# Kernel tuning notes

Measured on AMD Instinct MI355X. Metric: run time of the kernel, lower is better.

## Reference

```python
import jax, jax.numpy as jnp
import numpy as np

N = 65536
H = 512
E = 8
OUT = 2

def setup_inputs() -> dict:
    key = jax.random.key(0)
    ks = jax.random.split(key, 9)
    s = 0.1
    return {
        "x": jax.random.normal(ks[0], (N, 10), dtype=jnp.float32),
        "w1": jax.random.normal(ks[1], (H,), dtype=jnp.float32) * s,        # fc1: Linear(1,H) weight
        "b1": jax.random.normal(ks[2], (H,), dtype=jnp.float32) * s,
        "meta_w": jax.random.normal(ks[3], (E, H), dtype=jnp.float32) * s,  # 8 Linear(1,H) weights stacked
        "meta_b": jax.random.normal(ks[4], (E, H), dtype=jnp.float32) * s,
        "w2": jax.random.normal(ks[5], (H, H), dtype=jnp.float32) * s,      # fc2 weight (in,out layout)
        "b2": jax.random.normal(ks[6], (H,), dtype=jnp.float32) * s,
        "w3": jax.random.normal(ks[7], (H, OUT), dtype=jnp.float32) * s,    # fc3 weight
        "b3": jax.random.normal(ks[8], (OUT,), dtype=jnp.float32) * s,
    }

def reference(x, w1, b1, meta_w, meta_b, w2, b2, w3, b3):
    one_hot = x[:, 0:8]          # [N,8] expert combine weights
    delta = x[:, 8:9]            # [N,1]
    phi = x[:, 9:10]             # [N,1]
    # fc1(delta): Linear with input_dim=1 -> outer product with weight column
    x1 = delta * w1[None, :] + b1[None, :]                       # [N,H]
    # Per-expert Linear(1,H) on phi, combined with one_hot. Since each expert
    # is linear in phi, the dense [N,H,8] tensor + matmul of the original
    # collapses exactly to: phi * (one_hot @ meta_w) + one_hot @ meta_b.
    x2 = phi * (one_hot @ meta_w) + one_hot @ meta_b             # [N,H]
    h = jax.nn.relu(x1 + x2)
    h = jax.nn.relu(h @ w2 + b2)
    return h @ w3 + b3                                           # [N,OUT]
```

## Files before the change

kernel.cpp:

```cpp
#include <hip/hip_runtime.h>


#define BM 64

typedef float f32x4 __attribute__((ext_vector_type(4)));
typedef short s16x8 __attribute__((ext_vector_type(8)));

__device__ __forceinline__ short f2bf(float f) {
    union { float f; unsigned u; } c; c.f = f;
    unsigned u = c.u;
    return (short)((u + 0x7FFFu + ((u >> 16) & 1u)) >> 16);
}

__global__ void prep_kernel(const float* __restrict__ w1, const float* __restrict__ b1,
                            const float* __restrict__ mw, const float* __restrict__ mb,
                            const float* __restrict__ w2,
                            short* __restrict__ w2s, short* __restrict__ waugS) {
    int id = blockIdx.x * 256 + threadIdx.x;
    if (id < 512 * 512) {
        int k = id / 512, n = id % 512;
        int ks = k >> 5, g = (k >> 3) & 3, j = k & 7;
        w2s[(((ks * 4 + g) * 512) + n) * 8 + j] = f2bf(w2[id]);
    }
    if (id < 512 * 32) {
        int col = id >> 5, k = id & 31;
        float v = 0.f;
        if (k < 8)        v = mw[k * 512 + col];
        else if (k < 16)  v = mb[(k - 8) * 512 + col];
        else if (k == 16) v = w1[col];
        else if (k == 17) v = b1[col];
        waugS[col * 32 + k] = f2bf(v);
    }
}

__global__ __launch_bounds__(512, 4) void fused_mlp(
    const float* __restrict__ x, const short* __restrict__ waugS,
    const short* __restrict__ w2s, const float* __restrict__ b2,
    const float* __restrict__ w3, const float* __restrict__ b3,
    float* __restrict__ out) {

    __shared__ __align__(16) short haug[64 * 512];
    __shared__ float xls[64 * 10];
    __shared__ float oacc[128];

    const int tid  = threadIdx.x;
    const int wv   = tid >> 6;
    const int lane = tid & 63;
    const int l15  = lane & 15;
    const int g    = lane >> 4;
    const long rowbase = (long)blockIdx.x * BM;

    for (int i = tid; i < BM * 10; i += 512) xls[i] = x[rowbase * 10 + i];
    if (tid < 128) oacc[tid] = 0.f;
    __syncthreads();

    {
        s16x8 afr[4];
#pragma unroll
        for (int m = 0; m < 4; ++m) {
            int r = m * 16 + l15;
            float v[8];
            if (g == 0) {
                float phi = xls[r * 10 + 9];
#pragma unroll
                for (int j = 0; j < 8; ++j) v[j] = xls[r * 10 + j] * phi;
            } else if (g == 1) {
#pragma unroll
                for (int j = 0; j < 8; ++j) v[j] = xls[r * 10 + j];
            } else if (g == 2) {
                v[0] = xls[r * 10 + 8]; v[1] = 1.f;
#pragma unroll
                for (int j = 2; j < 8; ++j) v[j] = 0.f;
            } else {
#pragma unroll
                for (int j = 0; j < 8; ++j) v[j] = 0.f;
            }
            s16x8 a;
#pragma unroll
            for (int j = 0; j < 8; ++j) a[j] = f2bf(v[j]);
            afr[m] = a;
        }
#pragma unroll
        for (int nf = 0; nf < 4; ++nf) {
            int col = wv * 64 + nf * 16 + l15;
            s16x8 bfr = *(const s16x8*)(waugS + col * 32 + g * 8);
            int chi = (col >> 3) * 512 + (col & 7);
#pragma unroll
            for (int m = 0; m < 4; ++m) {
                f32x4 c = {0.f, 0.f, 0.f, 0.f};
                c = __builtin_amdgcn_mfma_f32_16x16x32_bf16(afr[m], bfr, c, 0, 0, 0);
#pragma unroll
                for (int r4 = 0; r4 < 4; ++r4) {
                    int row = m * 16 + g * 4 + r4;
                    float hv = c[r4];
                    hv = hv > 0.f ? hv : 0.f;
                    haug[chi + row * 8] = f2bf(hv);
                }
            }
        }
    }
    __syncthreads();

    f32x4 acc[4][4];
#pragma unroll
    for (int m = 0; m < 4; ++m)
#pragma unroll
        for (int n = 0; n < 4; ++n) acc[m][n] = (f32x4){0.f, 0.f, 0.f, 0.f};

    const char* bfp = (const char*)w2s + g * 8192 + (wv * 64 + l15) * 16;
    const char* hbp = (const char*)haug + g * 1024 + l15 * 16;

#define LOADB(dst, T)                                                  \
    do {                                                               \
        dst[0] = *(const s16x8*)(bfp + (size_t)(T) * 32768);           \
        dst[1] = *(const s16x8*)(bfp + (size_t)(T) * 32768 + 256);     \
        dst[2] = *(const s16x8*)(bfp + (size_t)(T) * 32768 + 512);     \
        dst[3] = *(const s16x8*)(bfp + (size_t)(T) * 32768 + 768);     \
    } while (0)

#define DOSTEP(bfv)                                                                          \
    do {                                                                                     \
        s16x8 a0 = *(const s16x8*)(hbp);                                                     \
        s16x8 a1 = *(const s16x8*)(hbp + 256);                                               \
        s16x8 a2 = *(const s16x8*)(hbp + 512);                                               \
        s16x8 a3 = *(const s16x8*)(hbp + 768);                                               \
        acc[0][0] = __builtin_amdgcn_mfma_f32_16x16x32_bf16(a0, bfv[0], acc[0][0], 0, 0, 0); \
        acc[0][1] = __builtin_amdgcn_mfma_f32_16x16x32_bf16(a0, bfv[1], acc[0][1], 0, 0, 0); \
        acc[0][2] = __builtin_amdgcn_mfma_f32_16x16x32_bf16(a0, bfv[2], acc[0][2], 0, 0, 0); \
        acc[0][3] = __builtin_amdgcn_mfma_f32_16x16x32_bf16(a0, bfv[3], acc[0][3], 0, 0, 0); \
        acc[1][0] = __builtin_amdgcn_mfma_f32_16x16x32_bf16(a1, bfv[0], acc[1][0], 0, 0, 0); \
        acc[1][1] = __builtin_amdgcn_mfma_f32_16x16x32_bf16(a1, bfv[1], acc[1][1], 0, 0, 0); \
        acc[1][2] = __builtin_amdgcn_mfma_f32_16x16x32_bf16(a1, bfv[2], acc[1][2], 0, 0, 0); \
        acc[1][3] = __builtin_amdgcn_mfma_f32_16x16x32_bf16(a1, bfv[3], acc[1][3], 0, 0, 0); \
        acc[2][0] = __builtin_amdgcn_mfma_f32_16x16x32_bf16(a2, bfv[0], acc[2][0], 0, 0, 0); \
        acc[2][1] = __builtin_amdgcn_mfma_f32_16x16x32_bf16(a2, bfv[1], acc[2][1], 0, 0, 0); \
        acc[2][2] = __builtin_amdgcn_mfma_f32_16x16x32_bf16(a2, bfv[2], acc[2][2], 0, 0, 0); \
        acc[2][3] = __builtin_amdgcn_mfma_f32_16x16x32_bf16(a2, bfv[3], acc[2][3], 0, 0, 0); \
        acc[3][0] = __builtin_amdgcn_mfma_f32_16x16x32_bf16(a3, bfv[0], acc[3][0], 0, 0, 0); \
        acc[3][1] = __builtin_amdgcn_mfma_f32_16x16x32_bf16(a3, bfv[1], acc[3][1], 0, 0, 0); \
        acc[3][2] = __builtin_amdgcn_mfma_f32_16x16x32_bf16(a3, bfv[2], acc[3][2], 0, 0, 0); \
        acc[3][3] = __builtin_amdgcn_mfma_f32_16x16x32_bf16(a3, bfv[3], acc[3][3], 0, 0, 0); \
        hbp += 4096;                                                                         \
    } while (0)

    s16x8 bfA[4], bfB[4];
    LOADB(bfA, 0);

#pragma unroll 1
    for (int tt = 0; tt < 7; ++tt) {
        LOADB(bfB, 2 * tt + 1);
        DOSTEP(bfA);
        LOADB(bfA, 2 * tt + 2);
        DOSTEP(bfB);
    }
    LOADB(bfB, 15);
    DOSTEP(bfA);
    DOSTEP(bfB);

#undef LOADB
#undef DOSTEP

    float bb2[4], w30[4], w31[4];
#pragma unroll
    for (int n = 0; n < 4; ++n) {
        int col = wv * 64 + n * 16 + l15;
        bb2[n] = b2[col];
        w30[n] = w3[col * 2 + 0];
        w31[n] = w3[col * 2 + 1];
    }
#pragma unroll
    for (int m = 0; m < 4; ++m) {
#pragma unroll
        for (int r4 = 0; r4 < 4; ++r4) {
            float s0 = 0.f, s1 = 0.f;
#pragma unroll
            for (int n = 0; n < 4; ++n) {
                float v = acc[m][n][r4] + bb2[n];
                v = v > 0.f ? v : 0.f;
                s0 += v * w30[n];
                s1 += v * w31[n];
            }
            s0 += __shfl_xor(s0, 1); s1 += __shfl_xor(s1, 1);
            s0 += __shfl_xor(s0, 2); s1 += __shfl_xor(s1, 2);
            s0 += __shfl_xor(s0, 4); s1 += __shfl_xor(s1, 4);
            s0 += __shfl_xor(s0, 8); s1 += __shfl_xor(s1, 8);
            if (l15 == 0) {
                int row = m * 16 + g * 4 + r4;
                atomicAdd(&oacc[row * 2 + 0], s0);
                atomicAdd(&oacc[row * 2 + 1], s1);
            }
        }
    }
    __syncthreads();

    if (tid < 128) {
        int row = tid >> 1, o = tid & 1;
        out[(rowbase + row) * 2 + o] = oacc[tid] + b3[o];
    }
}

extern "C" void kernel_launch(void* const* d_in, const int* in_sizes, int n_in,
                              void* d_out, int out_size, void* d_ws, size_t ws_size,
                              hipStream_t stream) {
    const float* x  = (const float*)d_in[0];
    const float* w1 = (const float*)d_in[1];
    const float* b1 = (const float*)d_in[2];
    const float* mw = (const float*)d_in[3];
    const float* mb = (const float*)d_in[4];
    const float* w2 = (const float*)d_in[5];
    const float* b2 = (const float*)d_in[6];
    const float* w3 = (const float*)d_in[7];
    const float* b3 = (const float*)d_in[8];
    float* out = (float*)d_out;

    short* w2s   = (short*)d_ws;
    short* waugS = w2s + 512 * 512;

    prep_kernel<<<1024, 256, 0, stream>>>(w1, b1, mw, mb, w2, w2s, waugS);
    fused_mlp<<<65536 / BM, 512, 0, stream>>>(x, waugS, w2s, b2, w3, b3, out);
}
```

Baseline: 57.66 us.

## Double row tile to 128 per block to reuse W2 fragments across more rows

Raises the block row tile from 64 to 128, doubling the LDS hidden buffer and the per-wave accumulator count to 8x4 MFMA tiles. Each W2 fragment loaded from global or L2 is now applied to twice as many rows, halving total weight traffic per output row. The cost is higher register and LDS use: launch bounds drop to 2 blocks per CU, the LDS layout stride changes, and there are half as many blocks, which lowers occupancy and latency hiding.

```diff
diff --git a/kernel.cpp b/kernel.cpp
--- a/kernel.cpp
+++ b/kernel.cpp
@@ -1,7 +1,7 @@
 #include <hip/hip_runtime.h>
 
 
-#define BM 64
+#define BM 128
 
 typedef float f32x4 __attribute__((ext_vector_type(4)));
 typedef short s16x8 __attribute__((ext_vector_type(8)));
@@ -33,15 +33,15 @@
     }
 }
 
-__global__ __launch_bounds__(512, 4) void fused_mlp(
+__global__ __launch_bounds__(512, 2) void fused_mlp(
     const float* __restrict__ x, const short* __restrict__ waugS,
     const short* __restrict__ w2s, const float* __restrict__ b2,
     const float* __restrict__ w3, const float* __restrict__ b3,
     float* __restrict__ out) {
 
-    __shared__ __align__(16) short haug[64 * 512];
-    __shared__ float xls[64 * 10];
-    __shared__ float oacc[128];
+    __shared__ __align__(16) short haug[128 * 512];
+    __shared__ float xls[128 * 10];
+    __shared__ float oacc[256];
 
     const int tid  = threadIdx.x;
     const int wv   = tid >> 6;
@@ -51,13 +51,18 @@
     const long rowbase = (long)blockIdx.x * BM;
 
     for (int i = tid; i < BM * 10; i += 512) xls[i] = x[rowbase * 10 + i];
-    if (tid < 128) oacc[tid] = 0.f;
+    if (tid < 256) oacc[tid] = 0.f;
     __syncthreads();
 
     {
-        s16x8 afr[4];
-#pragma unroll
-        for (int m = 0; m < 4; ++m) {
+        s16x8 bfr[4];
+#pragma unroll
+        for (int nf = 0; nf < 4; ++nf) {
+            int col = wv * 64 + nf * 16 + l15;
+            bfr[nf] = *(const s16x8*)(waugS + col * 32 + g * 8);
+        }
+#pragma unroll
+        for (int m = 0; m < 8; ++m) {
             int r = m * 16 + l15;
             float v[8];
             if (g == 0) {
@@ -78,17 +83,12 @@
             s16x8 a;
 #pragma unroll
             for (int j = 0; j < 8; ++j) a[j] = f2bf(v[j]);
-            afr[m] = a;
-        }
-#pragma unroll
-        for (int nf = 0; nf < 4; ++nf) {
-            int col = wv * 64 + nf * 16 + l15;
-            s16x8 bfr = *(const s16x8*)(waugS + col * 32 + g * 8);
-            int chi = (col >> 3) * 512 + (col & 7);
-#pragma unroll
-            for (int m = 0; m < 4; ++m) {
+#pragma unroll
+            for (int nf = 0; nf < 4; ++nf) {
+                int col = wv * 64 + nf * 16 + l15;
+                int chi = (col >> 3) * 1024 + (col & 7);
                 f32x4 c = {0.f, 0.f, 0.f, 0.f};
-                c = __builtin_amdgcn_mfma_f32_16x16x32_bf16(afr[m], bfr, c, 0, 0, 0);
+                c = __builtin_amdgcn_mfma_f32_16x16x32_bf16(a, bfr[nf], c, 0, 0, 0);
 #pragma unroll
                 for (int r4 = 0; r4 < 4; ++r4) {
                     int row = m * 16 + g * 4 + r4;
@@ -101,14 +101,14 @@
     }
     __syncthreads();
 
-    f32x4 acc[4][4];
-#pragma unroll
-    for (int m = 0; m < 4; ++m)
+    f32x4 acc[8][4];
+#pragma unroll
+    for (int m = 0; m < 8; ++m)
 #pragma unroll
         for (int n = 0; n < 4; ++n) acc[m][n] = (f32x4){0.f, 0.f, 0.f, 0.f};
 
     const char* bfp = (const char*)w2s + g * 8192 + (wv * 64 + l15) * 16;
-    const char* hbp = (const char*)haug + g * 1024 + l15 * 16;
+    const char* hbp = (const char*)haug + g * 2048 + l15 * 16;
 
 #define LOADB(dst, T)                                                  \
     do {                                                               \
@@ -118,30 +118,31 @@
         dst[3] = *(const s16x8*)(bfp + (size_t)(T) * 32768 + 768);     \
     } while (0)
 
-#define DOSTEP(bfv)                                                                          \
-    do {                                                                                     \
-        s16x8 a0 = *(const s16x8*)(hbp);                                                     \
-        s16x8 a1 = *(const s16x8*)(hbp + 256);                                               \
-        s16x8 a2 = *(const s16x8*)(hbp + 512);                                               \
-        s16x8 a3 = *(const s16x8*)(hbp + 768);                                               \
-        acc[0][0] = __builtin_amdgcn_mfma_f32_16x16x32_bf16(a0, bfv[0], acc[0][0], 0, 0, 0); \
-        acc[0][1] = __builtin_amdgcn_mfma_f32_16x16x32_bf16(a0, bfv[1], acc[0][1], 0, 0, 0); \
-        acc[0][2] = __builtin_amdgcn_mfma_f32_16x16x32_bf16(a0, bfv[2], acc[0][2], 0, 0, 0); \
-        acc[0][3] = __builtin_amdgcn_mfma_f32_16x16x32_bf16(a0, bfv[3], acc[0][3], 0, 0, 0); \
-        acc[1][0] = __builtin_amdgcn_mfma_f32_16x16x32_bf16(a1, bfv[0], acc[1][0], 0, 0, 0); \
-        acc[1][1] = __builtin_amdgcn_mfma_f32_16x16x32_bf16(a1, bfv[1], acc[1][1], 0, 0, 0); \
-        acc[1][2] = __builtin_amdgcn_mfma_f32_16x16x32_bf16(a1, bfv[2], acc[1][2], 0, 0, 0); \
-        acc[1][3] = __builtin_amdgcn_mfma_f32_16x16x32_bf16(a1, bfv[3], acc[1][3], 0, 0, 0); \
-        acc[2][0] = __builtin_amdgcn_mfma_f32_16x16x32_bf16(a2, bfv[0], acc[2][0], 0, 0, 0); \
-        acc[2][1] = __builtin_amdgcn_mfma_f32_16x16x32_bf16(a2, bfv[1], acc[2][1], 0, 0, 0); \
-        acc[2][2] = __builtin_amdgcn_mfma_f32_16x16x32_bf16(a2, bfv[2], acc[2][2], 0, 0, 0); \
-        acc[2][3] = __builtin_amdgcn_mfma_f32_16x16x32_bf16(a2, bfv[3], acc[2][3], 0, 0, 0); \
-        acc[3][0] = __builtin_amdgcn_mfma_f32_16x16x32_bf16(a3, bfv[0], acc[3][0], 0, 0, 0); \
-        acc[3][1] = __builtin_amdgcn_mfma_f32_16x16x32_bf16(a3, bfv[1], acc[3][1], 0, 0, 0); \
-        acc[3][2] = __builtin_amdgcn_mfma_f32_16x16x32_bf16(a3, bfv[2], acc[3][2], 0, 0, 0); \
-        acc[3][3] = __builtin_amdgcn_mfma_f32_16x16x32_bf16(a3, bfv[3], acc[3][3], 0, 0, 0); \
-        hbp += 4096;                                                                         \
+#define HALF(bfv, MB)                                                                            \
+    do {                                                                                         \
+        s16x8 a0 = *(const s16x8*)(hbp + (MB) * 1024);                                           \
+        s16x8 a1 = *(const s16x8*)(hbp + (MB) * 1024 + 256);                                     \
+        s16x8 a2 = *(const s16x8*)(hbp + (MB) * 1024 + 512);                                     \
+        s16x8 a3 = *(const s16x8*)(hbp + (MB) * 1024 + 768);                                     \
+        acc[(MB)*4+0][0] = __builtin_amdgcn_mfma_f32_16x16x32_bf16(a0, bfv[0], acc[(MB)*4+0][0], 0, 0, 0); \
+        acc[(MB)*4+0][1] = __builtin_amdgcn_mfma_f32_16x16x32_bf16(a0, bfv[1], acc[(MB)*4+0][1], 0, 0, 0); \
+        acc[(MB)*4+0][2] = __builtin_amdgcn_mfma_f32_16x16x32_bf16(a0, bfv[2], acc[(MB)*4+0][2], 0, 0, 0); \
+        acc[(MB)*4+0][3] = __builtin_amdgcn_mfma_f32_16x16x32_bf16(a0, bfv[3], acc[(MB)*4+0][3], 0, 0, 0); \
+        acc[(MB)*4+1][0] = __builtin_amdgcn_mfma_f32_16x16x32_bf16(a1, bfv[0], acc[(MB)*4+1][0], 0, 0, 0); \
+        acc[(MB)*4+1][1] = __builtin_amdgcn_mfma_f32_16x16x32_bf16(a1, bfv[1], acc[(MB)*4+1][1], 0, 0, 0); \
+        acc[(MB)*4+1][2] = __builtin_amdgcn_mfma_f32_16x16x32_bf16(a1, bfv[2], acc[(MB)*4+1][2], 0, 0, 0); \
+        acc[(MB)*4+1][3] = __builtin_amdgcn_mfma_f32_16x16x32_bf16(a1, bfv[3], acc[(MB)*4+1][3], 0, 0, 0); \
+        acc[(MB)*4+2][0] = __builtin_amdgcn_mfma_f32_16x16x32_bf16(a2, bfv[0], acc[(MB)*4+2][0], 0, 0, 0); \
+        acc[(MB)*4+2][1] = __builtin_amdgcn_mfma_f32_16x16x32_bf16(a2, bfv[1], acc[(MB)*4+2][1], 0, 0, 0); \
+        acc[(MB)*4+2][2] = __builtin_amdgcn_mfma_f32_16x16x32_bf16(a2, bfv[2], acc[(MB)*4+2][2], 0, 0, 0); \
+        acc[(MB)*4+2][3] = __builtin_amdgcn_mfma_f32_16x16x32_bf16(a2, bfv[3], acc[(MB)*4+2][3], 0, 0, 0); \
+        acc[(MB)*4+3][0] = __builtin_amdgcn_mfma_f32_16x16x32_bf16(a3, bfv[0], acc[(MB)*4+3][0], 0, 0, 0); \
+        acc[(MB)*4+3][1] = __builtin_amdgcn_mfma_f32_16x16x32_bf16(a3, bfv[1], acc[(MB)*4+3][1], 0, 0, 0); \
+        acc[(MB)*4+3][2] = __builtin_amdgcn_mfma_f32_16x16x32_bf16(a3, bfv[2], acc[(MB)*4+3][2], 0, 0, 0); \
+        acc[(MB)*4+3][3] = __builtin_amdgcn_mfma_f32_16x16x32_bf16(a3, bfv[3], acc[(MB)*4+3][3], 0, 0, 0); \
     } while (0)
+
+#define DOSTEP(bfv) do { HALF(bfv, 0); HALF(bfv, 1); hbp += 8192; } while (0)
 
     s16x8 bfA[4], bfB[4];
     LOADB(bfA, 0);
@@ -158,6 +159,7 @@
     DOSTEP(bfB);
 
 #undef LOADB
+#undef HALF
 #undef DOSTEP
 
     float bb2[4], w30[4], w31[4];
@@ -169,7 +171,7 @@
         w31[n] = w3[col * 2 + 1];
     }
 #pragma unroll
-    for (int m = 0; m < 4; ++m) {
+    for (int m = 0; m < 8; ++m) {
 #pragma unroll
         for (int r4 = 0; r4 < 4; ++r4) {
             float s0 = 0.f, s1 = 0.f;
@@ -193,7 +195,7 @@
     }
     __syncthreads();
 
-    if (tid < 128) {
+    if (tid < 256) {
         int row = tid >> 1, o = tid & 1;
         out[(rowbase + row) * 2 + o] = oacc[tid] + b3[o];
     }
```

Measured after the change: 59.37 us. 1.03x slower.
